# Kernel tuning notes

Measured on AMD Instinct MI355X. Metric: run time of the kernel, lower is better.

Reference implementation:

```python
import jax, jax.numpy as jnp
import numpy as np

B, N, E = 2, 2048, 2048
HQ, HKV, D = 32, 8, 64
SCALE = 1.0 / np.sqrt(D)


def setup_inputs() -> dict:
    key = jax.random.key(0)
    ks = jax.random.split(key, 9)
    s = lambda k, shape, fan: jax.random.normal(k, shape, jnp.float32) / np.sqrt(fan)
    return {
        "x": jax.random.normal(ks[0], (B, N, E), jnp.float32),
        "Wq": s(ks[1], (HQ * D, E), E),
        "bq": jnp.zeros((HQ * D,), jnp.float32),
        "Wk": s(ks[2], (HKV * D, E), E),
        "bk": jnp.zeros((HKV * D,), jnp.float32),
        "Wv": s(ks[3], (HKV * D, E), E),
        "bv": jnp.zeros((HKV * D,), jnp.float32),
        "Wo": s(ks[4], (E, E), E),
        "bo": jnp.zeros((E,), jnp.float32),
    }


def _attention(x, Wq, bq, Wk, bk, Wv, bv, Wo, bo):
    G = HQ // HKV  # query heads per kv head
    # projections (torch Linear: y = x @ W.T + b)
    q = (jnp.einsum("bne,fe->bnf", x, Wq) + bq).reshape(B, N, HKV, G, D)
    k = (jnp.einsum("bne,fe->bnf", x, Wk) + bk).reshape(B, N, HKV, D)
    v = (jnp.einsum("bne,fe->bnf", x, Wv) + bv).reshape(B, N, HKV, D)
    # scores [B, HKV, G, N, N] -- GQA without materializing repeated K/V
    scores = jnp.einsum("bnhgd,bmhd->bhgnm", q, k) * SCALE
    causal = jnp.tril(jnp.ones((N, N), bool))
    scores = jnp.where(causal, scores, -jnp.inf)
    p = jax.nn.softmax(scores, axis=-1)
    o = jnp.einsum("bhgnm,bmhd->bnhgd", p, v).reshape(B, N, E)
    return jnp.einsum("bne,fe->bnf", o, Wo) + bo


def reference(x, Wq, bq, Wk, bk, Wv, bv, Wo, bo):
    return _attention(x, Wq, bq, Wk, bk, Wv, bv, Wo, bo)
```

## Files before the change

kernel.cpp:

```cpp
#include <hip/hip_runtime.h>
#include <hip/hip_bf16.h>


#define B_   2
#define N_   2048
#define E_   2048
#define HQ_  32
#define HKV_ 8
#define D_   64
#define BN_  (B_*N_)

typedef __attribute__((ext_vector_type(8))) short bf16x8;
typedef __attribute__((ext_vector_type(4))) float f32x4;

#define MFMA16(a,b,c) __builtin_amdgcn_mfma_f32_16x16x32_bf16(a,b,c,0,0,0)

__device__ inline unsigned short f2bf(float f) {
  unsigned u = __builtin_bit_cast(unsigned, f);
  u += 0x7FFFu + ((u >> 16) & 1u);
  return (unsigned short)(u >> 16);
}

__device__ inline void gload_lds16(const void* g, void* l) {
  __builtin_amdgcn_global_load_lds(
      (const __attribute__((address_space(1))) void*)g,
      (__attribute__((address_space(3))) void*)l, 16, 0, 0);
}

__global__ void cast_all(const float* __restrict__ x,  const float* __restrict__ wq,
                         const float* __restrict__ wk, const float* __restrict__ wv,
                         const float* __restrict__ wo, unsigned short* __restrict__ dst) {
  const int c0 = 2097152;
  const int c1 = c0 + 1048576;
  const int c2 = c1 + 262144;
  const int c3 = c2 + 262144;
  const int c4 = c3 + 1048576;
  int i = blockIdx.x * blockDim.x + threadIdx.x;
  const int stride = gridDim.x * blockDim.x;
  for (; i < c4; i += stride) {
    const float* src; int off;
    if      (i < c0) { src = x;  off = i; }
    else if (i < c1) { src = wq; off = i - c0; }
    else if (i < c2) { src = wk; off = i - c1; }
    else if (i < c3) { src = wv; off = i - c2; }
    else             { src = wo; off = i - c3; }
    float4 f = reinterpret_cast<const float4*>(src)[off];
    ushort4 u;
    u.x = f2bf(f.x); u.y = f2bf(f.y); u.z = f2bf(f.z); u.w = f2bf(f.w);
    reinterpret_cast<ushort4*>(dst)[i] = u;
  }
}

__global__ __launch_bounds__(512, 2) void gemm_qkv(
    const unsigned short* __restrict__ A,
    const unsigned short* __restrict__ Wq, const unsigned short* __restrict__ Wk,
    const unsigned short* __restrict__ Wv,
    const float* __restrict__ bq, const float* __restrict__ bk, const float* __restrict__ bv,
    unsigned short* __restrict__ Qo, unsigned short* __restrict__ Ko,
    unsigned short* __restrict__ Vto)
{
  __shared__ __align__(16) unsigned short As[2][2][8192];
  __shared__ __align__(16) unsigned short Bs[2][2][8192];
  const int tid  = threadIdx.x;
  const int w    = tid >> 6;
  const int lane = tid & 63;
  const int g    = blockIdx.x & 7;
  const int s    = blockIdx.x >> 3;
  const int bm   = g*2 + (s >= 12);
  const int bn   = (s >= 12) ? (s - 12) : s;
  const int m0   = bm << 8;
  const int n0v  = bn << 8;
  const int K    = E_;

  const unsigned short* W; const float* bias; int wn0, seg;
  if      (n0v < 2048) { W = Wq; bias = bq; wn0 = n0v;        seg = 0; }
  else if (n0v < 2560) { W = Wk; bias = bk; wn0 = n0v - 2048; seg = 1; }
  else                 { W = Wv; bias = bv; wn0 = n0v - 2560; seg = 2; }

  const int mr   = w >> 2;
  const int nc   = w & 3;
  const int cl   = lane & 15;
  const int kgrp = lane >> 4;
  const int rl   = kgrp << 2;
  const int li   = lane >> 3;
  const int lx   = lane & 7;

  const unsigned gsw = ((unsigned)(lx ^ li)) << 3;
  const unsigned short* gA[2]; const unsigned short* gB[2];
  #pragma unroll
  for (int h = 0; h < 2; ++h) {
    gA[h] = A + (size_t)(m0  + h*128 + w*16 + li) * K + gsw;
    gB[h] = W + (size_t)(wn0 + h*128 + w*16 + li) * K + gsw;
  }
  const unsigned ldso = (unsigned)(w*16)*64u + (unsigned)lane*8u;
  const unsigned rsw  = (unsigned)(cl & 7);

  f32x4 acc[8][4] = {};
  const int nt = K >> 6;

  auto STAGE_P = [&](int kt, int buf, int h) {
    const int ko = kt << 6;
    #pragma unroll
    for (int q = 0; q < 2; ++q)
      gload_lds16(gA[h] + (size_t)(q*8)*K + ko, &As[buf][h][ldso + q*512]);
    #pragma unroll
    for (int q = 0; q < 2; ++q)
      gload_lds16(gB[h] + (size_t)(q*8)*K + ko, &Bs[buf][h][ldso + q*512]);
  };

  STAGE_P(0, 0, 0); STAGE_P(0, 0, 1);
  STAGE_P(1, 1, 0); STAGE_P(1, 1, 1);
  asm volatile("s_waitcnt vmcnt(8)" ::: "memory");
  __builtin_amdgcn_s_barrier();

  for (int t = 0; t < nt; ++t) {
    const int p = t & 1;
    const unsigned short* Ah = As[p][mr];
    const unsigned short* Bh = Bs[p][nc >> 1];
    bf16x8 bfr[4];
    #pragma unroll
    for (int ph = 0; ph < 4; ++ph) {
      const int ks = ph >> 1, mq = ph & 1;
      bf16x8 af[4];
      #pragma unroll
      for (int z = 0; z < 4; ++z) {
        const unsigned row = (unsigned)(mq*64 + z*16 + cl);
        af[z] = *reinterpret_cast<const bf16x8*>(
            &Ah[row*64u + ((((unsigned)(ks*4 + kgrp)) ^ rsw) << 3)]);
      }
      if ((ph & 1) == 0) {
        #pragma unroll
        for (int jj = 0; jj < 4; ++jj) {
          const unsigned row = (unsigned)((nc & 1)*64 + jj*16 + cl);
          bfr[jj] = *reinterpret_cast<const bf16x8*>(
              &Bh[row*64u + ((((unsigned)(ks*4 + kgrp)) ^ rsw) << 3)]);
        }
      }
      if (ph < 2 && t >= 1 && t + 1 < nt) STAGE_P(t + 1, p ^ 1, ph);
      __builtin_amdgcn_s_barrier();
      __builtin_amdgcn_s_setprio(1);
      #pragma unroll
      for (int z = 0; z < 4; ++z)
        #pragma unroll
        for (int jj = 0; jj < 4; ++jj)
          acc[mq*4 + z][jj] = MFMA16(af[z], bfr[jj], acc[mq*4 + z][jj]);
      __builtin_amdgcn_s_setprio(0);
      if (ph == 3) asm volatile("s_waitcnt vmcnt(0)" ::: "memory");
      __builtin_amdgcn_s_barrier();
    }
  }

  #pragma unroll
  for (int mi = 0; mi < 8; ++mi) {
    const int rowb = m0 + mr*128 + (mi >> 2)*64 + (mi & 3)*16 + rl;
    #pragma unroll
    for (int jj = 0; jj < 4; ++jj) {
      const int col = wn0 + nc*64 + jj*16 + cl;
      const float bj = bias[col];
      if (seg == 0) {
        #pragma unroll
        for (int r = 0; r < 4; ++r)
          Qo[(size_t)(rowb + r) * 2048 + col] = f2bf(acc[mi][jj][r] + bj);
      } else if (seg == 1) {
        #pragma unroll
        for (int r = 0; r < 4; ++r)
          Ko[(size_t)(rowb + r) * 512 + col] = f2bf(acc[mi][jj][r] + bj);
      } else {
        ushort4 u;
        u.x = f2bf(acc[mi][jj][0] + bj);
        u.y = f2bf(acc[mi][jj][1] + bj);
        u.z = f2bf(acc[mi][jj][2] + bj);
        u.w = f2bf(acc[mi][jj][3] + bj);
        *reinterpret_cast<ushort4*>(&Vto[(size_t)col * 4096 + rowb]) = u;
      }
    }
  }
}

__global__ __launch_bounds__(256) void gemm_out(
    const unsigned short* __restrict__ A, const unsigned short* __restrict__ W,
    const float* __restrict__ bias, float* __restrict__ C)
{
  __shared__ __align__(16) unsigned short As[128*64];
  __shared__ __align__(16) unsigned short Bs[128*64];
  const int tid  = threadIdx.x;
  const int w    = tid >> 6;
  const int lane = tid & 63;
  const int bm   = blockIdx.x >> 4;
  const int bn   = blockIdx.x & 15;
  const int m0   = bm << 7, n0 = bn << 7;
  const int K    = E_;
  const int wr   = (w >> 1) << 6;
  const int wc   = (w & 1) << 6;
  const int cl   = lane & 15;
  const int kgrp = lane >> 4;
  const int rl   = kgrp << 2;
  const int li   = lane >> 3;
  const int lx   = lane & 7;

  const unsigned schunk = ((unsigned)(lx ^ li)) << 3;
  const unsigned short* gA = A + (size_t)(m0 + li) * K + schunk;
  const unsigned short* gB = W + (size_t)(n0 + li) * K + schunk;
  unsigned short* lA = As + lane*8;
  unsigned short* lB = Bs + lane*8;

  unsigned rA[4][2], rB[4][2];
  #pragma unroll
  for (int z = 0; z < 4; ++z)
    #pragma unroll
    for (int ks = 0; ks < 2; ++ks) {
      rA[z][ks] = (unsigned)(wr + z*16 + cl)*64u + ((((unsigned)ks*4u + (unsigned)kgrp) ^ (unsigned)(cl & 7)) << 3);
      rB[z][ks] = (unsigned)(wc + z*16 + cl)*64u + ((((unsigned)ks*4u + (unsigned)kgrp) ^ (unsigned)(cl & 7)) << 3);
    }

  f32x4 acc[4][4] = {};

  for (int kt = 0; kt < (K >> 6); ++kt) {
    const int ko = kt << 6;
    #pragma unroll
    for (int q = 0; q < 4; ++q) {
      const unsigned i = (unsigned)(w*4 + q);
      gload_lds16(gA + ((size_t)i*8*K + ko), lA + i*512);
      gload_lds16(gB + ((size_t)i*8*K + ko), lB + i*512);
    }
    __syncthreads();
    #pragma unroll
    for (int ks = 0; ks < 2; ++ks) {
      bf16x8 af[4], bfr[4];
      #pragma unroll
      for (int i = 0; i < 4; ++i)
        af[i] = *reinterpret_cast<const bf16x8*>(&As[rA[i][ks]]);
      #pragma unroll
      for (int j = 0; j < 4; ++j)
        bfr[j] = *reinterpret_cast<const bf16x8*>(&Bs[rB[j][ks]]);
      #pragma unroll
      for (int i = 0; i < 4; ++i)
        #pragma unroll
        for (int j = 0; j < 4; ++j)
          acc[i][j] = MFMA16(af[i], bfr[j], acc[i][j]);
    }
    __syncthreads();
  }

  #pragma unroll
  for (int j = 0; j < 4; ++j) {
    const int col = n0 + wc + j*16 + cl;
    const float bj = bias[col];
    #pragma unroll
    for (int i = 0; i < 4; ++i) {
      const int row = m0 + wr + i*16 + rl;
      #pragma unroll
      for (int r = 0; r < 4; ++r)
        C[(size_t)(row + r) * E_ + col] = acc[i][j][r] + bj;
    }
  }
}

__global__ __launch_bounds__(256, 2) void attn_kernel(
    const unsigned short* __restrict__ Q, const unsigned short* __restrict__ K,
    const unsigned short* __restrict__ Vt, unsigned short* __restrict__ O)
{
  __shared__ __align__(16) unsigned short Kbuf[2][4096];
  __shared__ __align__(16) unsigned short Vbuf[2][4096];
  __shared__ __align__(16) unsigned short Ps[4][2048];
  const int tid  = threadIdx.x;
  const int w    = tid >> 6;
  const int lane = tid & 63;
  const int bh   = blockIdx.x;
  const int b    = bh >> 3;
  const int h    = bh & 7;
  const int j    = blockIdx.y;
  const int hq   = h*4 + w;
  const int cl   = lane & 15;
  const int kgrp = lane >> 4;
  const int rl   = kgrp << 2;
  const int li   = lane >> 3;
  const int lx   = lane & 7;

  const float K2 = 0.125f * 1.44269504088896340736f;

  char* pws = (char*)&Ps[w][0];
  const unsigned swz = ((unsigned)(cl & 7)) << 4;

  bf16x8 ones8;
  #pragma unroll
  for (int q = 0; q < 8; ++q) ones8[q] = (short)0x3F80;

  const char* Kp = (const char*)(K + (size_t)(b*N_)*512 + h*64);
  const char* Vp = (const char*)(Vt + (size_t)(h*64)*BN_ + b*N_);

  const unsigned schunk = ((unsigned)(lx ^ li)) << 4;
  const unsigned kso  = (unsigned)li*1024u + schunk;
  const unsigned vso  = (unsigned)li*8192u + schunk;
  const unsigned ldst = (unsigned)lane*16u;

  unsigned rdo[4][2];
  #pragma unroll
  for (int z = 0; z < 4; ++z)
    #pragma unroll
    for (int ks = 0; ks < 2; ++ks)
      rdo[z][ks] = (unsigned)z*2048u + (unsigned)cl*128u
                 + ((((unsigned)ks*4u + (unsigned)kgrp) ^ (unsigned)(cl & 7)) << 4);

  unsigned wb[2][4], rb[2][2];
  #pragma unroll
  for (int i = 0; i < 2; ++i) {
    #pragma unroll
    for (int c = 0; c < 4; ++c)
      wb[i][c] = (unsigned)i*2048u + (unsigned)cl*128u
               + (((unsigned)c*32u + (unsigned)kgrp*8u) ^ swz);
    #pragma unroll
    for (int ks = 0; ks < 2; ++ks)
      rb[i][ks] = (unsigned)i*2048u + (unsigned)cl*128u
                + (((unsigned)ks*64u + (unsigned)kgrp*16u) ^ swz);
  }

  for (int sp = 0; sp < 2; ++sp) {
    __syncthreads();
    const int sidx = sp ? (63 - j) : j;
    const int q0   = sidx << 5;
    const int nt   = (sidx >> 1) + 1;

    bf16x8 qf[2][2];
    #pragma unroll
    for (int i = 0; i < 2; ++i) {
      const size_t qoff = (size_t)(b*N_ + q0 + i*16 + cl) * E_ + hq*64 + (kgrp << 3);
      qf[i][0] = *reinterpret_cast<const bf16x8*>(Q + qoff);
      qf[i][1] = *reinterpret_cast<const bf16x8*>(Q + qoff + 32);
    }

    f32x4 o[2][4] = {};
    f32x4 l4[2] = {};
    float m[2] = {-1e30f, -1e30f};

    #pragma unroll
    for (int q = 0; q < 2; ++q) {
      const unsigned i = (unsigned)(w*2 + q);
      gload_lds16(Kp + (i*8192u + kso),  (char*)Kbuf[0] + (i*1024u + ldst));
      gload_lds16(Vp + (i*65536u + vso), (char*)Vbuf[0] + (i*1024u + ldst));
    }
    int cur = 0;
    __syncthreads();

    for (int t = 0; t < nt; ++t) {
      if (t + 1 < nt) {
        const unsigned kt = (unsigned)(t + 1) * 65536u;
        const unsigned vt = (unsigned)(t + 1) * 128u;
        #pragma unroll
        for (int q = 0; q < 2; ++q) {
          const unsigned i = (unsigned)(w*2 + q);
          gload_lds16(Kp + (kt + i*8192u + kso),  (char*)Kbuf[cur^1] + (i*1024u + ldst));
          gload_lds16(Vp + (vt + i*65536u + vso), (char*)Vbuf[cur^1] + (i*1024u + ldst));
        }
      }

      bf16x8 kf[4][2];
      #pragma unroll
      for (int c = 0; c < 4; ++c)
        #pragma unroll
        for (int ks = 0; ks < 2; ++ks)
          kf[c][ks] = *reinterpret_cast<const bf16x8*>((const char*)Kbuf[cur] + rdo[c][ks]);

      f32x4 s[2][4];
      #pragma unroll
      for (int i = 0; i < 2; ++i)
        #pragma unroll
        for (int c = 0; c < 4; ++c) {
          f32x4 z = {};
          z = MFMA16(kf[c][0], qf[i][0], z);
          z = MFMA16(kf[c][1], qf[i][1], z);
          s[i][c] = z;
        }

      if (t == nt - 1) {
        const int kvb = t << 6;
        #pragma unroll
        for (int i = 0; i < 2; ++i) {
          const int qq = q0 + i*16 + cl;
          #pragma unroll
          for (int c = 0; c < 4; ++c)
            #pragma unroll
            for (int r = 0; r < 4; ++r)
              if (kvb + c*16 + rl + r > qq) s[i][c][r] = -1e30f;
        }
      }

      #pragma unroll
      for (int i = 0; i < 2; ++i) {
        float t0 = fmaxf(fmaxf(s[i][0][0], s[i][0][1]), fmaxf(s[i][0][2], s[i][0][3]));
        float t1 = fmaxf(fmaxf(s[i][1][0], s[i][1][1]), fmaxf(s[i][1][2], s[i][1][3]));
        float t2 = fmaxf(fmaxf(s[i][2][0], s[i][2][1]), fmaxf(s[i][2][2], s[i][2][3]));
        float t3 = fmaxf(fmaxf(s[i][3][0], s[i][3][1]), fmaxf(s[i][3][2], s[i][3][3]));
        float tm = fmaxf(fmaxf(t0, t1), fmaxf(t2, t3));
        tm = fmaxf(tm, __shfl_xor(tm, 16, 64));
        tm = fmaxf(tm, __shfl_xor(tm, 32, 64));
        const float mn = fmaxf(m[i], tm);
        const float al = __builtin_amdgcn_exp2f(K2 * (m[i] - mn));
        m[i] = mn;
        l4[i] *= al;
        #pragma unroll
        for (int db = 0; db < 4; ++db) o[i][db] *= al;
        #pragma unroll
        for (int c = 0; c < 4; ++c) {
          ushort4 u;
          u.x = f2bf(__builtin_amdgcn_exp2f(K2 * (s[i][c][0] - mn)));
          u.y = f2bf(__builtin_amdgcn_exp2f(K2 * (s[i][c][1] - mn)));
          u.z = f2bf(__builtin_amdgcn_exp2f(K2 * (s[i][c][2] - mn)));
          u.w = f2bf(__builtin_amdgcn_exp2f(K2 * (s[i][c][3] - mn)));
          *reinterpret_cast<ushort4*>(pws + wb[i][c]) = u;
        }
      }

      bf16x8 vf[4][2];
      #pragma unroll
      for (int db = 0; db < 4; ++db)
        #pragma unroll
        for (int ks = 0; ks < 2; ++ks)
          vf[db][ks] = *reinterpret_cast<const bf16x8*>((const char*)Vbuf[cur] + rdo[db][ks]);

      #pragma unroll
      for (int i = 0; i < 2; ++i) {
        const bf16x8 pa0 = *reinterpret_cast<const bf16x8*>(pws + rb[i][0]);
        const bf16x8 pa1 = *reinterpret_cast<const bf16x8*>(pws + rb[i][1]);
        l4[i] = MFMA16(ones8, pa0, l4[i]);
        l4[i] = MFMA16(ones8, pa1, l4[i]);
        #pragma unroll
        for (int db = 0; db < 4; ++db) {
          o[i][db] = MFMA16(vf[db][0], pa0, o[i][db]);
          o[i][db] = MFMA16(vf[db][1], pa1, o[i][db]);
        }
      }

      __syncthreads();
      cur ^= 1;
    }

    #pragma unroll
    for (int i = 0; i < 2; ++i) {
      const float inv = 1.0f / l4[i][0];
      const size_t orow = (size_t)(b*N_ + q0 + i*16 + cl) * E_ + hq*64 + rl;
      #pragma unroll
      for (int db = 0; db < 4; ++db) {
        ushort4 u;
        u.x = f2bf(o[i][db][0] * inv);
        u.y = f2bf(o[i][db][1] * inv);
        u.z = f2bf(o[i][db][2] * inv);
        u.w = f2bf(o[i][db][3] * inv);
        *reinterpret_cast<ushort4*>(&O[orow + db*16]) = u;
      }
    }
  }
}

extern "C" void kernel_launch(void* const* d_in, const int* in_sizes, int n_in,
                              void* d_out, int out_size, void* d_ws, size_t ws_size,
                              hipStream_t stream) {
  const float* x  = (const float*)d_in[0];
  const float* Wq = (const float*)d_in[1];
  const float* bq = (const float*)d_in[2];
  const float* Wk = (const float*)d_in[3];
  const float* bk = (const float*)d_in[4];
  const float* Wv = (const float*)d_in[5];
  const float* bv = (const float*)d_in[6];
  const float* Wo = (const float*)d_in[7];
  const float* bo = (const float*)d_in[8];
  float* out = (float*)d_out;

  unsigned short* ws  = (unsigned short*)d_ws;
  unsigned short* xb  = ws;
  unsigned short* Wqb = xb  + 8388608;
  unsigned short* Wkb = Wqb + 4194304;
  unsigned short* Wvb = Wkb + 1048576;
  unsigned short* Wob = Wvb + 1048576;
  unsigned short* Qb  = Wob + 4194304;
  unsigned short* Kb  = Qb  + 8388608;
  unsigned short* Vtb = Kb  + 2097152;
  unsigned short* Ob  = Vtb + 2097152;

  cast_all<<<dim3(2048), dim3(256), 0, stream>>>(x, Wq, Wk, Wv, Wo, xb);

  gemm_qkv<<<dim3(192), dim3(512), 0, stream>>>(xb, Wqb, Wkb, Wvb,
                                                bq, bk, bv, Qb, Kb, Vtb);

  attn_kernel<<<dim3(16, 32), dim3(256), 0, stream>>>(Qb, Kb, Vtb, Ob);

  gemm_out<<<dim3(32*16), dim3(256), 0, stream>>>(Ob, Wob, bo, out);
}
```

Baseline: 195.3 us.

## Restructure QKV GEMM staging into K-half LDS slices with finer pipelining

Reorganizes the QKV projection GEMM so each LDS buffer holds a 32-wide K half of the full 256-row A and B tiles, rather than 128-row halves with 64-wide K. The next tile's half is issued before the current half is computed, using vmcnt-based waits and one barrier per half. The LDS read offsets and XOR swizzle are precomputed per thread, and the occupancy hint of two blocks per SM is removed from launch bounds. This aims to overlap global-to-LDS loads with MFMA work and cut per-phase barriers and address arithmetic. In exchange it changes the bank-conflict swizzle pattern and relies on correct vmcnt accounting with a single barrier per stage.

```diff
diff --git a/kernel.cpp b/kernel.cpp
--- a/kernel.cpp
+++ b/kernel.cpp
@@ -51,7 +51,7 @@
   }
 }
 
-__global__ __launch_bounds__(512, 2) void gemm_qkv(
+__global__ __launch_bounds__(512) void gemm_qkv(
     const unsigned short* __restrict__ A,
     const unsigned short* __restrict__ Wq, const unsigned short* __restrict__ Wk,
     const unsigned short* __restrict__ Wv,
@@ -62,8 +62,8 @@
   __shared__ __align__(16) unsigned short As[2][2][8192];
   __shared__ __align__(16) unsigned short Bs[2][2][8192];
   const int tid  = threadIdx.x;
+  const int lane = tid & 63;
   const int w    = tid >> 6;
-  const int lane = tid & 63;
   const int g    = blockIdx.x & 7;
   const int s    = blockIdx.x >> 3;
   const int bm   = g*2 + (s >= 12);
@@ -82,71 +82,73 @@
   const int cl   = lane & 15;
   const int kgrp = lane >> 4;
   const int rl   = kgrp << 2;
-  const int li   = lane >> 3;
-  const int lx   = lane & 7;
-
-  const unsigned gsw = ((unsigned)(lx ^ li)) << 3;
-  const unsigned short* gA[2]; const unsigned short* gB[2];
-  #pragma unroll
-  for (int h = 0; h < 2; ++h) {
-    gA[h] = A + (size_t)(m0  + h*128 + w*16 + li) * K + gsw;
-    gB[h] = W + (size_t)(wn0 + h*128 + w*16 + li) * K + gsw;
-  }
-  const unsigned ldso = (unsigned)(w*16)*64u + (unsigned)lane*8u;
-  const unsigned rsw  = (unsigned)(cl & 7);
+
+  const int srow = tid >> 2;
+  const unsigned sch = ((unsigned)((tid & 3) ^ (srow & 3))) << 3;
+  const unsigned short* gAb = A + (size_t)(m0  + srow) * K + sch;
+  const unsigned short* gBb = W + (size_t)(wn0 + srow) * K + sch;
+  const unsigned ldse = (unsigned)tid * 8u;
+
+  const unsigned rch = ((unsigned)(kgrp ^ (cl & 3))) << 3;
+  unsigned rAo[2][4], rBo[4];
+  #pragma unroll
+  for (int mq = 0; mq < 2; ++mq)
+    #pragma unroll
+    for (int z = 0; z < 4; ++z)
+      rAo[mq][z] = (unsigned)(mr*128 + mq*64 + z*16 + cl) * 32u + rch;
+  #pragma unroll
+  for (int jj = 0; jj < 4; ++jj)
+    rBo[jj] = (unsigned)(nc*64 + jj*16 + cl) * 32u + rch;
 
   f32x4 acc[8][4] = {};
   const int nt = K >> 6;
 
-  auto STAGE_P = [&](int kt, int buf, int h) {
-    const int ko = kt << 6;
+  auto STAGE = [&](int kt, int buf, int kh) {
+    const int ko = (kt << 6) + (kh << 5);
     #pragma unroll
     for (int q = 0; q < 2; ++q)
-      gload_lds16(gA[h] + (size_t)(q*8)*K + ko, &As[buf][h][ldso + q*512]);
+      gload_lds16(gAb + (size_t)(q*128)*K + ko, &As[buf][kh][ldse + q*4096u]);
     #pragma unroll
     for (int q = 0; q < 2; ++q)
-      gload_lds16(gB[h] + (size_t)(q*8)*K + ko, &Bs[buf][h][ldso + q*512]);
+      gload_lds16(gBb + (size_t)(q*128)*K + ko, &Bs[buf][kh][ldse + q*4096u]);
   };
 
-  STAGE_P(0, 0, 0); STAGE_P(0, 0, 1);
-  STAGE_P(1, 1, 0); STAGE_P(1, 1, 1);
-  asm volatile("s_waitcnt vmcnt(8)" ::: "memory");
-  __builtin_amdgcn_s_barrier();
+  STAGE(0, 0, 0);
+  STAGE(0, 0, 1);
 
   for (int t = 0; t < nt; ++t) {
     const int p = t & 1;
-    const unsigned short* Ah = As[p][mr];
-    const unsigned short* Bh = Bs[p][nc >> 1];
-    bf16x8 bfr[4];
-    #pragma unroll
-    for (int ph = 0; ph < 4; ++ph) {
-      const int ks = ph >> 1, mq = ph & 1;
-      bf16x8 af[4];
-      #pragma unroll
-      for (int z = 0; z < 4; ++z) {
-        const unsigned row = (unsigned)(mq*64 + z*16 + cl);
-        af[z] = *reinterpret_cast<const bf16x8*>(
-            &Ah[row*64u + ((((unsigned)(ks*4 + kgrp)) ^ rsw) << 3)]);
-      }
-      if ((ph & 1) == 0) {
-        #pragma unroll
-        for (int jj = 0; jj < 4; ++jj) {
-          const unsigned row = (unsigned)((nc & 1)*64 + jj*16 + cl);
-          bfr[jj] = *reinterpret_cast<const bf16x8*>(
-              &Bh[row*64u + ((((unsigned)(ks*4 + kgrp)) ^ rsw) << 3)]);
-        }
-      }
-      if (ph < 2 && t >= 1 && t + 1 < nt) STAGE_P(t + 1, p ^ 1, ph);
+    #pragma unroll
+    for (int ks = 0; ks < 2; ++ks) {
+      if (t + 1 < nt) {
+        STAGE(t + 1, p ^ 1, ks);
+        asm volatile("s_waitcnt vmcnt(8)" ::: "memory");
+      } else if (ks == 0) {
+        asm volatile("s_waitcnt vmcnt(4)" ::: "memory");
+      } else {
+        asm volatile("s_waitcnt vmcnt(0)" ::: "memory");
+      }
       __builtin_amdgcn_s_barrier();
-      __builtin_amdgcn_s_setprio(1);
-      #pragma unroll
-      for (int z = 0; z < 4; ++z)
-        #pragma unroll
-        for (int jj = 0; jj < 4; ++jj)
-          acc[mq*4 + z][jj] = MFMA16(af[z], bfr[jj], acc[mq*4 + z][jj]);
-      __builtin_amdgcn_s_setprio(0);
-      if (ph == 3) asm volatile("s_waitcnt vmcnt(0)" ::: "memory");
-      __builtin_amdgcn_s_barrier();
+      const unsigned short* Ah = As[p][ks];
+      const unsigned short* Bh = Bs[p][ks];
+      bf16x8 bfr[4];
+      #pragma unroll
+      for (int jj = 0; jj < 4; ++jj)
+        bfr[jj] = *reinterpret_cast<const bf16x8*>(&Bh[rBo[jj]]);
+      #pragma unroll
+      for (int mq = 0; mq < 2; ++mq) {
+        bf16x8 af[4];
+        #pragma unroll
+        for (int z = 0; z < 4; ++z)
+          af[z] = *reinterpret_cast<const bf16x8*>(&Ah[rAo[mq][z]]);
+        __builtin_amdgcn_s_setprio(1);
+        #pragma unroll
+        for (int z = 0; z < 4; ++z)
+          #pragma unroll
+          for (int jj = 0; jj < 4; ++jj)
+            acc[mq*4 + z][jj] = MFMA16(af[z], bfr[jj], acc[mq*4 + z][jj]);
+        __builtin_amdgcn_s_setprio(0);
+      }
     }
   }
 
```

Result: no change. 196.6 us (+0.7%).

## Double-buffer output GEMM with larger tiles and simplify QKV GEMM prefetch pipeline

Applied to the files above, without the earlier changes.

The output projection GEMM moves from 256-thread 128x128 tiles with a synchronous load-then-compute loop to 512-thread 256x128 tiles. It double-buffers LDS with async global-to-LDS prefetch of the next K tile, uses an XCD-aware block mapping, and raises MFMA priority. The QKV GEMM drops its phase-interleaved staging for a simpler per-iteration prefetch of the next tile with a single wait and barrier pair, and loosens its launch bounds from two blocks per CU. The goal is to hide global load latency and cut barrier count, at the cost of more LDS per block and possibly lower occupancy or less fine-grained overlap in the QKV kernel.

```diff
diff --git a/kernel.cpp b/kernel.cpp
--- a/kernel.cpp
+++ b/kernel.cpp
@@ -51,7 +51,7 @@
   }
 }
 
-__global__ __launch_bounds__(512, 2) void gemm_qkv(
+__global__ __launch_bounds__(512) void gemm_qkv(
     const unsigned short* __restrict__ A,
     const unsigned short* __restrict__ Wq, const unsigned short* __restrict__ Wk,
     const unsigned short* __restrict__ Wv,
@@ -109,45 +109,48 @@
   };
 
   STAGE_P(0, 0, 0); STAGE_P(0, 0, 1);
-  STAGE_P(1, 1, 0); STAGE_P(1, 1, 1);
-  asm volatile("s_waitcnt vmcnt(8)" ::: "memory");
-  __builtin_amdgcn_s_barrier();
+  int p = 0;
 
   for (int t = 0; t < nt; ++t) {
-    const int p = t & 1;
+    if (t + 1 < nt) {
+      STAGE_P(t + 1, p ^ 1, 0);
+      STAGE_P(t + 1, p ^ 1, 1);
+      asm volatile("s_waitcnt vmcnt(8)" ::: "memory");
+    } else {
+      asm volatile("s_waitcnt vmcnt(0)" ::: "memory");
+    }
+    __builtin_amdgcn_s_barrier();
     const unsigned short* Ah = As[p][mr];
     const unsigned short* Bh = Bs[p][nc >> 1];
-    bf16x8 bfr[4];
-    #pragma unroll
-    for (int ph = 0; ph < 4; ++ph) {
-      const int ks = ph >> 1, mq = ph & 1;
-      bf16x8 af[4];
-      #pragma unroll
-      for (int z = 0; z < 4; ++z) {
-        const unsigned row = (unsigned)(mq*64 + z*16 + cl);
-        af[z] = *reinterpret_cast<const bf16x8*>(
-            &Ah[row*64u + ((((unsigned)(ks*4 + kgrp)) ^ rsw) << 3)]);
-      }
-      if ((ph & 1) == 0) {
-        #pragma unroll
-        for (int jj = 0; jj < 4; ++jj) {
-          const unsigned row = (unsigned)((nc & 1)*64 + jj*16 + cl);
-          bfr[jj] = *reinterpret_cast<const bf16x8*>(
-              &Bh[row*64u + ((((unsigned)(ks*4 + kgrp)) ^ rsw) << 3)]);
+    #pragma unroll
+    for (int ks = 0; ks < 2; ++ks) {
+      bf16x8 bfr[4];
+      #pragma unroll
+      for (int jj = 0; jj < 4; ++jj) {
+        const unsigned row = (unsigned)((nc & 1)*64 + jj*16 + cl);
+        bfr[jj] = *reinterpret_cast<const bf16x8*>(
+            &Bh[row*64u + ((((unsigned)(ks*4 + kgrp)) ^ rsw) << 3)]);
+      }
+      #pragma unroll
+      for (int mq = 0; mq < 2; ++mq) {
+        bf16x8 af[4];
+        #pragma unroll
+        for (int z = 0; z < 4; ++z) {
+          const unsigned row = (unsigned)(mq*64 + z*16 + cl);
+          af[z] = *reinterpret_cast<const bf16x8*>(
+              &Ah[row*64u + ((((unsigned)(ks*4 + kgrp)) ^ rsw) << 3)]);
         }
-      }
-      if (ph < 2 && t >= 1 && t + 1 < nt) STAGE_P(t + 1, p ^ 1, ph);
-      __builtin_amdgcn_s_barrier();
-      __builtin_amdgcn_s_setprio(1);
-      #pragma unroll
-      for (int z = 0; z < 4; ++z)
-        #pragma unroll
-        for (int jj = 0; jj < 4; ++jj)
-          acc[mq*4 + z][jj] = MFMA16(af[z], bfr[jj], acc[mq*4 + z][jj]);
-      __builtin_amdgcn_s_setprio(0);
-      if (ph == 3) asm volatile("s_waitcnt vmcnt(0)" ::: "memory");
-      __builtin_amdgcn_s_barrier();
-    }
+        __builtin_amdgcn_s_setprio(1);
+        #pragma unroll
+        for (int z = 0; z < 4; ++z)
+          #pragma unroll
+          for (int jj = 0; jj < 4; ++jj)
+            acc[mq*4 + z][jj] = MFMA16(af[z], bfr[jj], acc[mq*4 + z][jj]);
+        __builtin_amdgcn_s_setprio(0);
+      }
+    }
+    __builtin_amdgcn_s_barrier();
+    p ^= 1;
   }
 
   #pragma unroll
@@ -177,18 +180,20 @@
   }
 }
 
-__global__ __launch_bounds__(256) void gemm_out(
+__global__ __launch_bounds__(512) void gemm_out(
     const unsigned short* __restrict__ A, const unsigned short* __restrict__ W,
     const float* __restrict__ bias, float* __restrict__ C)
 {
-  __shared__ __align__(16) unsigned short As[128*64];
-  __shared__ __align__(16) unsigned short Bs[128*64];
+  __shared__ __align__(16) unsigned short As[2][16384];
+  __shared__ __align__(16) unsigned short Bs[2][8192];
   const int tid  = threadIdx.x;
   const int w    = tid >> 6;
   const int lane = tid & 63;
-  const int bm   = blockIdx.x >> 4;
-  const int bn   = blockIdx.x & 15;
-  const int m0   = bm << 7, n0 = bn << 7;
+  const int g    = blockIdx.x & 7;
+  const int s    = blockIdx.x >> 3;
+  const int bm   = g*2 + (s >> 4);
+  const int bn   = s & 15;
+  const int m0   = bm << 8, n0 = bn << 7;
   const int K    = E_;
   const int wr   = (w >> 1) << 6;
   const int wc   = (w & 1) << 6;
@@ -199,59 +204,76 @@
   const int lx   = lane & 7;
 
   const unsigned schunk = ((unsigned)(lx ^ li)) << 3;
-  const unsigned short* gA = A + (size_t)(m0 + li) * K + schunk;
-  const unsigned short* gB = W + (size_t)(n0 + li) * K + schunk;
-  unsigned short* lA = As + lane*8;
-  unsigned short* lB = Bs + lane*8;
-
-  unsigned rA[4][2], rB[4][2];
+  const unsigned short* gA = A + (size_t)(m0 + w*32 + li) * K + schunk;
+  const unsigned short* gB = W + (size_t)(n0 + w*16 + li) * K + schunk;
+  const unsigned lA0 = (unsigned)(w*32)*64u + (unsigned)lane*8u;
+  const unsigned lB0 = (unsigned)(w*16)*64u + (unsigned)lane*8u;
+
+  unsigned rAo[4][2], rBo[4][2];
   #pragma unroll
   for (int z = 0; z < 4; ++z)
     #pragma unroll
     for (int ks = 0; ks < 2; ++ks) {
-      rA[z][ks] = (unsigned)(wr + z*16 + cl)*64u + ((((unsigned)ks*4u + (unsigned)kgrp) ^ (unsigned)(cl & 7)) << 3);
-      rB[z][ks] = (unsigned)(wc + z*16 + cl)*64u + ((((unsigned)ks*4u + (unsigned)kgrp) ^ (unsigned)(cl & 7)) << 3);
+      const unsigned ch = (((unsigned)(ks*4 + kgrp)) ^ (unsigned)(cl & 7)) << 3;
+      rAo[z][ks] = (unsigned)(wr + z*16 + cl)*64u + ch;
+      rBo[z][ks] = (unsigned)(wc + z*16 + cl)*64u + ch;
     }
 
   f32x4 acc[4][4] = {};
-
-  for (int kt = 0; kt < (K >> 6); ++kt) {
+  const int nt = K >> 6;
+
+  auto STAGE = [&](int kt, int buf) {
     const int ko = kt << 6;
     #pragma unroll
-    for (int q = 0; q < 4; ++q) {
-      const unsigned i = (unsigned)(w*4 + q);
-      gload_lds16(gA + ((size_t)i*8*K + ko), lA + i*512);
-      gload_lds16(gB + ((size_t)i*8*K + ko), lB + i*512);
-    }
-    __syncthreads();
+    for (int q = 0; q < 4; ++q)
+      gload_lds16(gA + (size_t)(q*8)*K + ko, &As[buf][lA0 + q*512]);
+    #pragma unroll
+    for (int q = 0; q < 2; ++q)
+      gload_lds16(gB + (size_t)(q*8)*K + ko, &Bs[buf][lB0 + q*512]);
+  };
+
+  STAGE(0, 0);
+  int p = 0;
+
+  for (int t = 0; t < nt; ++t) {
+    if (t + 1 < nt) {
+      STAGE(t + 1, p ^ 1);
+      asm volatile("s_waitcnt vmcnt(6)" ::: "memory");
+    } else {
+      asm volatile("s_waitcnt vmcnt(0)" ::: "memory");
+    }
+    __builtin_amdgcn_s_barrier();
     #pragma unroll
     for (int ks = 0; ks < 2; ++ks) {
       bf16x8 af[4], bfr[4];
       #pragma unroll
-      for (int i = 0; i < 4; ++i)
-        af[i] = *reinterpret_cast<const bf16x8*>(&As[rA[i][ks]]);
-      #pragma unroll
-      for (int j = 0; j < 4; ++j)
-        bfr[j] = *reinterpret_cast<const bf16x8*>(&Bs[rB[j][ks]]);
-      #pragma unroll
-      for (int i = 0; i < 4; ++i)
-        #pragma unroll
-        for (int j = 0; j < 4; ++j)
-          acc[i][j] = MFMA16(af[i], bfr[j], acc[i][j]);
-    }
-    __syncthreads();
-  }
-
-  #pragma unroll
-  for (int j = 0; j < 4; ++j) {
-    const int col = n0 + wc + j*16 + cl;
+      for (int z = 0; z < 4; ++z)
+        af[z] = *reinterpret_cast<const bf16x8*>(&As[p][rAo[z][ks]]);
+      #pragma unroll
+      for (int jj = 0; jj < 4; ++jj)
+        bfr[jj] = *reinterpret_cast<const bf16x8*>(&Bs[p][rBo[jj][ks]]);
+      __builtin_amdgcn_s_setprio(1);
+      #pragma unroll
+      for (int z = 0; z < 4; ++z)
+        #pragma unroll
+        for (int jj = 0; jj < 4; ++jj)
+          acc[z][jj] = MFMA16(af[z], bfr[jj], acc[z][jj]);
+      __builtin_amdgcn_s_setprio(0);
+    }
+    __builtin_amdgcn_s_barrier();
+    p ^= 1;
+  }
+
+  #pragma unroll
+  for (int jj = 0; jj < 4; ++jj) {
+    const int col = n0 + wc + jj*16 + cl;
     const float bj = bias[col];
     #pragma unroll
-    for (int i = 0; i < 4; ++i) {
-      const int row = m0 + wr + i*16 + rl;
+    for (int z = 0; z < 4; ++z) {
+      const int row = m0 + wr + z*16 + rl;
       #pragma unroll
       for (int r = 0; r < 4; ++r)
-        C[(size_t)(row + r) * E_ + col] = acc[i][j][r] + bj;
+        C[(size_t)(row + r) * E_ + col] = acc[z][jj][r] + bj;
     }
   }
 }
@@ -484,5 +506,5 @@
 
   attn_kernel<<<dim3(16, 32), dim3(256), 0, stream>>>(Qb, Kb, Vtb, Ob);
 
-  gemm_out<<<dim3(32*16), dim3(256), 0, stream>>>(Ob, Wob, bo, out);
-}
+  gemm_out<<<dim3(256), dim3(512), 0, stream>>>(Ob, Wob, bo, out);
+}
```

New measurement: 204.5 us. 4.7% more time.
